# Kernel optimization log

Hardware: AMD Instinct MI355X
Metric: run time of the kernel (lower is better)

## Reference

```python
import jax, jax.numpy as jnp
import numpy as np

NEG_SLOPE = 0.2  # PyG GATConv default negative_slope
H, C = 4, 64     # heads, per-head channels


def gat_layer(x, src, dst, edge_attr, W, a_src, a_dst, We, a_e, b):
    """PyG-style GATConv with edge features, concat=True. src/dst include self loops."""
    N = x.shape[0]
    h = (x @ W).reshape(N, H, C)                      # [N,H,C]
    al_s = (h * a_src[None]).sum(-1)                  # [N,H]
    al_d = (h * a_dst[None]).sum(-1)                  # [N,H]
    eh = (edge_attr @ We).reshape(-1, H, C)           # [E,H,C]
    al_e = (eh * a_e[None]).sum(-1)                   # [E,H]
    alpha = jax.nn.leaky_relu(al_s[src] + al_d[dst] + al_e, NEG_SLOPE)  # [E,H]
    # softmax over incoming edges of each destination node
    m = jax.ops.segment_max(alpha, dst, num_segments=N)
    p = jnp.exp(alpha - m[dst])
    denom = jax.ops.segment_sum(p, dst, num_segments=N)
    w = p / (denom[dst] + 1e-16)                      # [E,H]
    msg = h[src] * w[..., None]                       # [E,H,C]
    out = jax.ops.segment_sum(msg, dst, num_segments=N)  # [N,H,C]
    return out.reshape(N, H * C) + b


def setup_inputs() -> dict:
    key = jax.random.key(0)
    ks = jax.random.split(key, 20)
    N, E = 50000, 800000
    s = 0.05
    inp = {
        'x': jax.random.normal(ks[0], (N, 5), jnp.float32),
        'edge_index': jax.random.randint(ks[1], (2, E), 0, N, jnp.int32),
        'edge_attr': jax.random.normal(ks[2], (E, 4), jnp.float32),
        'W0': jax.random.normal(ks[3], (5, 256), jnp.float32) * s,
        'a_src0': jax.random.normal(ks[4], (H, C), jnp.float32) * s,
        'a_dst0': jax.random.normal(ks[5], (H, C), jnp.float32) * s,
        'We0': jax.random.normal(ks[6], (4, 256), jnp.float32) * s,
        'a_e0': jax.random.normal(ks[7], (H, C), jnp.float32) * s,
        'b0': jnp.zeros((256,), jnp.float32),
        'W1': jax.random.normal(ks[8], (256, 256), jnp.float32) * s,
        'a_src1': jax.random.normal(ks[9], (H, C), jnp.float32) * s,
        'a_dst1': jax.random.normal(ks[10], (H, C), jnp.float32) * s,
        'We1': jax.random.normal(ks[11], (4, 256), jnp.float32) * s,
        'a_e1': jax.random.normal(ks[12], (H, C), jnp.float32) * s,
        'b1': jnp.zeros((256,), jnp.float32),
        'Wm1': jax.random.normal(ks[13], (768, 128), jnp.float32) * s,
        'bm1': jnp.zeros((128,), jnp.float32),
        'Wm2': jax.random.normal(ks[14], (128, 64), jnp.float32) * s,
        'bm2': jnp.zeros((64,), jnp.float32),
        'Wm3': jax.random.normal(ks[15], (64, 128), jnp.float32) * s,
        'bm3': jnp.zeros((128,), jnp.float32),
    }
    return inp


def reference(x, edge_index, edge_attr,
              W0, a_src0, a_dst0, We0, a_e0, b0,
              W1, a_src1, a_dst1, We1, a_e1, b1,
              Wm1, bm1, Wm2, bm2, Wm3, bm3):
    N = x.shape[0]
    # add self loops once; self-loop edge_attr = mean of edge_attr (PyG fill_value='mean')
    loops = jnp.arange(N, dtype=edge_index.dtype)
    src = jnp.concatenate([edge_index[0], loops])
    dst = jnp.concatenate([edge_index[1], loops])
    mean_ea = jnp.mean(edge_attr, axis=0, keepdims=True)
    ea = jnp.concatenate([edge_attr, jnp.broadcast_to(mean_ea, (N, edge_attr.shape[1]))], axis=0)

    h = gat_layer(x, src, dst, ea, W0, a_src0, a_dst0, We0, a_e0, b0)
    h = jax.nn.relu(h)  # dropout is identity in eval
    h = gat_layer(h, src, dst, ea, W1, a_src1, a_dst1, We1, a_e1, b1)

    mean_pool = jnp.mean(h, axis=0)                      # [256]
    max_pool = jnp.max(h, axis=0)                        # [256]
    att = jax.nn.softmax(jnp.sum(h * mean_pool[None], axis=1))  # [N]
    att_pool = jnp.sum(h * att[:, None], axis=0)         # [256]
    comb = jnp.concatenate([mean_pool, max_pool, att_pool])  # [768]

    z = jax.nn.relu(comb @ Wm1 + bm1)
    z = jax.nn.relu(z @ Wm2 + bm2)
    g = z @ Wm3 + bm3
    return g[None]  # [1,128]
```

## Files before the change

kernel.cpp:

```cpp
#include <hip/hip_runtime.h>
#include <hip/hip_fp16.h>
#include <type_traits>

static const long long N_ = 50000;
static const long long E_ = 800000;

typedef __attribute__((ext_vector_type(8))) short bf16x8;
typedef __attribute__((ext_vector_type(4))) float f32x4;

__device__ __forceinline__ float lrelu(float x){ return x >= 0.f ? x : 0.2f*x; }
__device__ __forceinline__ unsigned fkey(float x){
  unsigned u = __float_as_uint(x);
  return (u & 0x80000000u) ? ~u : (u | 0x80000000u);
}
__device__ __forceinline__ float unfkey(unsigned k){
  return __uint_as_float((k & 0x80000000u) ? (k & 0x7fffffffu) : ~k);
}

__global__ void k_sumea(const float* __restrict__ ea, float* __restrict__ sum_ea){
  __shared__ float lds[256];
  int t = threadIdx.x;
  long long total = E_*4;
  float s = 0.f;
  for (long long i = (long long)blockIdx.x*256 + t; i < total; i += (long long)gridDim.x*256)
    s += ea[i];
  lds[t] = s; __syncthreads();
  for (int st=128; st>=4; st>>=1){ if (t<st) lds[t] += lds[t+st]; __syncthreads(); }
  if (t<4) atomicAdd(&sum_ea[t], lds[t]);
}

__global__ void k_deg(const int* __restrict__ ei, int* __restrict__ deg){
  long long e = (long long)blockIdx.x*256 + threadIdx.x;
  if (e < E_) atomicAdd(&deg[ei[E_ + e]], 1);
}

__global__ void k_scan1(const int* __restrict__ deg, int* __restrict__ bsum){
  __shared__ int lds[256];
  int t = threadIdx.x;
  long long idx = (long long)blockIdx.x*256 + t;
  lds[t] = (idx < N_) ? deg[idx] : 0;
  __syncthreads();
  for (int st=128; st>=1; st>>=1){ if (t<st) lds[t] += lds[t+st]; __syncthreads(); }
  if (t==0) bsum[blockIdx.x] = lds[0];
}

__global__ void k_scan2(const int* __restrict__ bsum, int* __restrict__ bpre, int nb,
                        int* __restrict__ rowptr){
  __shared__ int lds[256];
  int t = threadIdx.x;
  int v = (t < nb) ? bsum[t] : 0;
  lds[t] = v; __syncthreads();
  for (int off=1; off<256; off<<=1){
    int add = (t>=off) ? lds[t-off] : 0;
    __syncthreads();
    lds[t] += add;
    __syncthreads();
  }
  if (t < nb) bpre[t] = lds[t] - v;
  if (t == 0) rowptr[N_] = (int)E_;
}

__global__ void k_scan3(const int* __restrict__ deg, const int* __restrict__ bpre,
                        int* __restrict__ rowptr, int* __restrict__ cursor){
  __shared__ int lds[256];
  int t = threadIdx.x;
  long long idx = (long long)blockIdx.x*256 + t;
  int v = (idx < N_) ? deg[idx] : 0;
  lds[t] = v; __syncthreads();
  for (int off=1; off<256; off<<=1){
    int add = (t>=off) ? lds[t-off] : 0;
    __syncthreads();
    lds[t] += add;
    __syncthreads();
  }
  if (idx < N_){
    int rp = bpre[blockIdx.x] + lds[t] - v;
    rowptr[idx] = rp; cursor[idx] = rp;
  }
}

__global__ void k_small(const float* __restrict__ We0, const float* __restrict__ ae0,
                        const float* __restrict__ We1, const float* __restrict__ ae1,
                        const float* __restrict__ sum_ea, float* __restrict__ small){
  int t = threadIdx.x;
  if (t < 32){
    int l = t>>4, f = (t>>2)&3, h = t&3;
    const float* We = l ? We1 : We0;
    const float* ae = l ? ae1 : ae0;
    float s = 0.f;
    for (int cc=0; cc<64; cc++) s += We[f*256 + h*64 + cc]*ae[h*64+cc];
    small[l*16 + f*4 + h] = s;
  }
  __syncthreads();
  if (t < 8){
    int l = t>>2, h = t&3;
    const float* Ae = small + l*16;
    const float invE = 1.f/(float)E_;
    float s = 0.f;
    for (int f=0; f<4; f++) s += sum_ea[f]*invE*Ae[f*4+h];
    small[32 + l*4 + h] = s;
  }
}

__global__ void k_scatter(const int* __restrict__ ei, const float* __restrict__ ea,
                          int* __restrict__ cursor, int* __restrict__ csr_src,
                          float* __restrict__ ale, const float* __restrict__ small){
  long long e = (long long)blockIdx.x*256 + threadIdx.x;
  if (e >= E_) return;
  int s = ei[e], d = ei[E_+e];
  int pos = atomicAdd(&cursor[d], 1);
  csr_src[pos] = s;
  float4 v = *(const float4*)(ea + e*4);
  float o0[4], o1[4];
  #pragma unroll
  for (int h=0; h<4; h++){
    o0[h] = v.x*small[0+h]  + v.y*small[4+h]  + v.z*small[8+h]  + v.w*small[12+h];
    o1[h] = v.x*small[16+h] + v.y*small[20+h] + v.z*small[24+h] + v.w*small[28+h];
  }
  float* p = ale + (long long)pos*8;
  *(float4*)(p)   = make_float4(o0[0],o0[1],o0[2],o0[3]);
  *(float4*)(p+4) = make_float4(o1[0],o1[1],o1[2],o1[3]);
}

__global__ void k_h0(const float* __restrict__ x, const float* __restrict__ W0,
                     const float* __restrict__ as0, const float* __restrict__ ad0,
                     __half* __restrict__ h0, float* __restrict__ als, float* __restrict__ ald){
  long long wid = ((long long)blockIdx.x*blockDim.x + threadIdx.x) >> 6;
  int lane = threadIdx.x & 63;
  if (wid >= N_) return;
  const float* xr = x + wid*5;
  float xv[5];
  #pragma unroll
  for (int f=0; f<5; f++) xv[f] = xr[f];
  int c = lane*4;
  float a0=0,a1=0,a2=0,a3=0;
  #pragma unroll
  for (int f=0; f<5; f++){
    const float* wr = W0 + f*256 + c;
    a0 += xv[f]*wr[0]; a1 += xv[f]*wr[1]; a2 += xv[f]*wr[2]; a3 += xv[f]*wr[3];
  }
  __half2 p01 = __floats2half2_rn(a0,a1);
  __half2 p23 = __floats2half2_rn(a2,a3);
  uint2 pk = make_uint2(*(unsigned*)&p01, *(unsigned*)&p23);
  *(uint2*)(h0 + wid*256 + c) = pk;
  const float* asp = as0 + c;
  const float* adp = ad0 + c;
  float ss = a0*asp[0]+a1*asp[1]+a2*asp[2]+a3*asp[3];
  float dd = a0*adp[0]+a1*adp[1]+a2*adp[2]+a3*adp[3];
  int head = lane>>4;
  #pragma unroll
  for (int m=1; m<16; m<<=1){ ss += __shfl_xor(ss, m); dd += __shfl_xor(dd, m); }
  if ((lane&15)==0){ als[wid*4+head]=ss; ald[wid*4+head]=dd; }
}

template<typename OutT, bool RELU>
__global__ void k_agg(const __half* __restrict__ hin, const float* __restrict__ als,
                      const float* __restrict__ ald, const int* __restrict__ rowptr,
                      const int* __restrict__ csr_src, const float* __restrict__ ale,
                      const float* __restrict__ small, int loop_off,
                      const float* __restrict__ bias, OutT* __restrict__ out){
  long long wid = ((long long)blockIdx.x*blockDim.x + threadIdx.x) >> 6;
  int lane = threadIdx.x & 63;
  if (wid >= N_) return;
  int head = lane>>4; int c = lane*4;
  float aldv = ald[wid*4+head];
  float a0 = lrelu(als[wid*4+head] + aldv + small[loop_off+head]);
  float m = a0, d = 1.f;
  uint2 pk0 = *(const uint2*)(hin + wid*256 + c);
  float2 f01 = __half22float2(*(__half2*)&pk0.x);
  float2 f23 = __half22float2(*(__half2*)&pk0.y);
  float accx=f01.x, accy=f01.y, accz=f23.x, accw=f23.y;
  int beg = rowptr[wid], end = rowptr[wid+1];
  int i = beg;
  for (; i+1 < end; i += 2){
    int s0 = csr_src[i], s1 = csr_src[i+1];
    float a1 = lrelu(als[(long long)s0*4+head] + aldv + ale[(long long)i*8+head]);
    float a2 = lrelu(als[(long long)s1*4+head] + aldv + ale[(long long)(i+1)*8+head]);
    uint2 pku = *(const uint2*)(hin + (long long)s0*256 + c);
    uint2 pkv = *(const uint2*)(hin + (long long)s1*256 + c);
    float2 u01=__half22float2(*(__half2*)&pku.x), u23=__half22float2(*(__half2*)&pku.y);
    float2 v01=__half22float2(*(__half2*)&pkv.x), v23=__half22float2(*(__half2*)&pkv.y);
    float nm = fmaxf(m, fmaxf(a1, a2));
    float sc = __expf(m - nm);
    float p1 = __expf(a1 - nm);
    float p2 = __expf(a2 - nm);
    d = d*sc + p1 + p2;
    accx = accx*sc + p1*u01.x + p2*v01.x;
    accy = accy*sc + p1*u01.y + p2*v01.y;
    accz = accz*sc + p1*u23.x + p2*v23.x;
    accw = accw*sc + p1*u23.y + p2*v23.y;
    m = nm;
  }
  if (i < end){
    int s0 = csr_src[i];
    float a = lrelu(als[(long long)s0*4+head] + aldv + ale[(long long)i*8+head]);
    uint2 pk = *(const uint2*)(hin + (long long)s0*256 + c);
    float2 g01=__half22float2(*(__half2*)&pk.x), g23=__half22float2(*(__half2*)&pk.y);
    float nm = fmaxf(m, a);
    float sc = __expf(m - nm);
    float p  = __expf(a - nm);
    d = d*sc + p;
    accx = accx*sc + p*g01.x;
    accy = accy*sc + p*g01.y;
    accz = accz*sc + p*g23.x;
    accw = accw*sc + p*g23.y;
    m = nm;
  }
  float inv = 1.f/(d + 1e-16f);
  const float* bp = bias + c;
  float ox = accx*inv + bp[0], oy = accy*inv + bp[1];
  float oz = accz*inv + bp[2], ow = accw*inv + bp[3];
  if (RELU){ ox=fmaxf(ox,0.f); oy=fmaxf(oy,0.f); oz=fmaxf(oz,0.f); ow=fmaxf(ow,0.f); }
  if constexpr (std::is_same<OutT,__half>::value){
    __half2 q01 = __floats2half2_rn(ox,oy);
    __half2 q23 = __floats2half2_rn(oz,ow);
    uint2 qk = make_uint2(*(unsigned*)&q01, *(unsigned*)&q23);
    *(uint2*)(out + wid*256 + c) = qk;
  } else {
    *(float4*)(out + wid*256 + c) = make_float4(ox,oy,oz,ow);
  }
}

__global__ void k_prepB(const float* __restrict__ W1, ushort* __restrict__ Bhi,
                        ushort* __restrict__ Blo){
  int k = blockIdx.x;
  int n = threadIdx.x;
  float v = W1[k*256+n];
  unsigned u = __float_as_uint(v);
  ushort hi = (ushort)(u>>16);
  float rem = v - __uint_as_float(u & 0xffff0000u);
  unsigned ur = __float_as_uint(rem);
  ushort lo = (ushort)((ur + 0x7fff + ((ur>>16)&1)) >> 16);
  int t = n>>4, kb = k>>5, q = (k>>3)&3, j = k&7;
  long long idx = ((((long long)t*8+kb)*64 + q*16 + (n&15))<<3) + j;
  Bhi[idx] = hi; Blo[idx] = lo;
}

__global__ __launch_bounds__(256) void k_gemm(const float* __restrict__ A,
    const ushort* __restrict__ Bhi, const ushort* __restrict__ Blo,
    __half* __restrict__ Ch, const float* __restrict__ as1, const float* __restrict__ ad1,
    float* __restrict__ als, float* __restrict__ ald){
  __shared__ ushort Ah[32*264];
  __shared__ ushort Al[32*264];
  int t = threadIdx.x;
  long long base = (long long)blockIdx.x*32;
  for (int i=t; i<2048; i+=256){
    int r = i>>6, q4 = i&63;
    float4 v = make_float4(0.f,0.f,0.f,0.f);
    if (base + r < N_) v = *(const float4*)(A + (base+r)*256 + q4*4);
    float vv[4] = {v.x,v.y,v.z,v.w};
    ushort hh[4], ll[4];
    #pragma unroll
    for (int e=0;e<4;e++){
      unsigned u = __float_as_uint(vv[e]);
      hh[e] = (ushort)(u>>16);
      float rem = vv[e] - __uint_as_float(u & 0xffff0000u);
      unsigned ur = __float_as_uint(rem);
      ll[e] = (ushort)((ur + 0x7fff + ((ur>>16)&1)) >> 16);
    }
    int off = r*264 + q4*4;
    *(ushort4*)(Ah+off) = make_ushort4(hh[0],hh[1],hh[2],hh[3]);
    *(ushort4*)(Al+off) = make_ushort4(ll[0],ll[1],ll[2],ll[3]);
  }
  __syncthreads();
  int w = t>>6, lane = t&63, m = lane&15, q = lane>>4;
  int rbase = (w>>1)*16;
  int nhalf = (w&1)*8;
  f32x4 acc[8];
  #pragma unroll
  for (int i=0;i<8;i++) acc[i] = (f32x4){0.f,0.f,0.f,0.f};
  for (int kb=0; kb<8; kb++){
    int aoff = (rbase+m)*264 + kb*32 + q*8;
    bf16x8 ah = *(const bf16x8*)(Ah + aoff);
    bf16x8 al = *(const bf16x8*)(Al + aoff);
    #pragma unroll
    for (int tt=0; tt<8; tt++){
      long long bidx = ((((long long)(nhalf+tt)*8+kb)*64 + lane)<<3);
      bf16x8 bh = *(const bf16x8*)(Bhi + bidx);
      bf16x8 bl = *(const bf16x8*)(Blo + bidx);
      acc[tt] = __builtin_amdgcn_mfma_f32_16x16x32_bf16(ah, bh, acc[tt], 0,0,0);
      acc[tt] = __builtin_amdgcn_mfma_f32_16x16x32_bf16(al, bh, acc[tt], 0,0,0);
      acc[tt] = __builtin_amdgcn_mfma_f32_16x16x32_bf16(ah, bl, acc[tt], 0,0,0);
    }
  }
  float ssv[4][2], ddv[4][2];
  #pragma unroll
  for (int r=0;r<4;r++){ ssv[r][0]=0.f; ssv[r][1]=0.f; ddv[r][0]=0.f; ddv[r][1]=0.f; }
  #pragma unroll
  for (int tt=0; tt<8; tt++){
    int col = (nhalf+tt)*16 + m;
    float as_ = as1[col], ad_ = ad1[col];
    int hh = tt>>2;
    #pragma unroll
    for (int r=0;r<4;r++){
      ssv[r][hh] += acc[tt][r]*as_;
      ddv[r][hh] += acc[tt][r]*ad_;
    }
  }
  #pragma unroll
  for (int r=0;r<4;r++){
    #pragma unroll
    for (int hh=0; hh<2; hh++){
      #pragma unroll
      for (int mm=1; mm<16; mm<<=1){
        ssv[r][hh] += __shfl_xor(ssv[r][hh], mm);
        ddv[r][hh] += __shfl_xor(ddv[r][hh], mm);
      }
    }
  }
  #pragma unroll
  for (int r=0;r<4;r++){
    long long grow = base + rbase + q*4 + r;
    if (grow < N_){
      #pragma unroll
      for (int tt=0; tt<8; tt++)
        Ch[grow*256 + (nhalf+tt)*16 + m] = __float2half(acc[tt][r]);
      if (m==0){
        int hb = (w&1)*2;
        als[grow*4 + hb+0] = ssv[r][0];
        ald[grow*4 + hb+0] = ddv[r][0];
        als[grow*4 + hb+1] = ssv[r][1];
        ald[grow*4 + hb+1] = ddv[r][1];
      }
    }
  }
}

__global__ void k_pool1(const __half* __restrict__ h2, float* __restrict__ sum_pool,
                        unsigned* __restrict__ maxkey){
  int c = threadIdx.x;
  float s = 0.f; float m = -3.4e38f;
  for (long long n = blockIdx.x; n < N_; n += gridDim.x){
    float v = __half2float(h2[n*256+c]); s += v; m = fmaxf(m, v);
  }
  atomicAdd(&sum_pool[c], s);
  atomicMax(&maxkey[c], fkey(m));
}

__global__ void k_atts(const __half* __restrict__ h2, const float* __restrict__ sum_pool,
                       float* __restrict__ sarr, unsigned* __restrict__ smax){
  __shared__ float lmax[4];
  int t = threadIdx.x; int lane = t&63; int w = t>>6;
  const float invN = 1.f/(float)N_;
  int c = lane*4;
  float4 mp = *(const float4*)(sum_pool + c);
  float mymax = -3.4e38f;
  for (long long wid = (long long)blockIdx.x*4 + w; wid < N_; wid += (long long)gridDim.x*4){
    uint2 pk = *(const uint2*)(h2 + wid*256 + c);
    float2 a01 = __half22float2(*(__half2*)&pk.x);
    float2 a23 = __half22float2(*(__half2*)&pk.y);
    float s = (a01.x*mp.x + a01.y*mp.y + a23.x*mp.z + a23.y*mp.w)*invN;
    #pragma unroll
    for (int m=1; m<64; m<<=1) s += __shfl_xor(s, m);
    if (lane==0) sarr[wid] = s;
    mymax = fmaxf(mymax, s);
  }
  if (lane==0) lmax[w] = mymax;
  __syncthreads();
  if (t==0){
    float mm = fmaxf(fmaxf(lmax[0],lmax[1]), fmaxf(lmax[2],lmax[3]));
    atomicMax(smax, fkey(mm));
  }
}

__global__ void k_attd(const float* __restrict__ sarr, const unsigned* __restrict__ smax,
                       float* __restrict__ ssum){
  __shared__ float lds[256];
  int t = threadIdx.x;
  float mx = unfkey(*smax);
  float s = 0.f;
  for (long long i = (long long)blockIdx.x*256 + t; i < N_; i += (long long)gridDim.x*256)
    s += __expf(sarr[i] - mx);
  lds[t] = s; __syncthreads();
  for (int st=128; st>=1; st>>=1){ if (t<st) lds[t]+=lds[t+st]; __syncthreads(); }
  if (t==0) atomicAdd(ssum, lds[0]);
}

__global__ void k_attp(const __half* __restrict__ h2, const float* __restrict__ sarr,
                       const unsigned* __restrict__ smax, const float* __restrict__ ssum,
                       float* __restrict__ att_pool){
  int c = threadIdx.x;
  float mx = unfkey(*smax);
  float inv = 1.f/(*ssum);
  float acc = 0.f;
  for (long long n = blockIdx.x; n < N_; n += gridDim.x){
    float w = __expf(sarr[n]-mx)*inv;
    acc += __half2float(h2[n*256+c])*w;
  }
  atomicAdd(&att_pool[c], acc);
}

__global__ void k_mlp(const float* __restrict__ sum_pool, const unsigned* __restrict__ maxkey,
                      const float* __restrict__ att_pool,
                      const float* __restrict__ Wm1, const float* __restrict__ bm1,
                      const float* __restrict__ Wm2, const float* __restrict__ bm2,
                      const float* __restrict__ Wm3, const float* __restrict__ bm3,
                      float* __restrict__ out){
  __shared__ float comb[768];
  __shared__ float z1p[4][128]; __shared__ float z1[128];
  __shared__ float z2p[8][64];  __shared__ float z2[64];
  __shared__ float z3p[4][128];
  int t = threadIdx.x;
  const float invN = 1.f/(float)N_;
  for (int i=t; i<768; i+=512){
    float v;
    if (i < 256)      v = sum_pool[i]*invN;
    else if (i < 512) v = unfkey(maxkey[i-256]);
    else              v = att_pool[i-512];
    comb[i] = v;
  }
  __syncthreads();
  { int n = t&127, part = t>>7;
    float a = 0.f;
    for (int f=part*192; f<part*192+192; f++) a += comb[f]*Wm1[f*128+n];
    z1p[part][n] = a;
  }
  __syncthreads();
  if (t < 128)
    z1[t] = fmaxf(bm1[t] + z1p[0][t]+z1p[1][t]+z1p[2][t]+z1p[3][t], 0.f);
  __syncthreads();
  { int n = t&63, part = t>>6;
    float a = 0.f;
    for (int f=part*16; f<part*16+16; f++) a += z1[f]*Wm2[f*64+n];
    z2p[part][n] = a;
  }
  __syncthreads();
  if (t < 64){
    float a = bm2[t];
    #pragma unroll
    for (int p=0;p<8;p++) a += z2p[p][t];
    z2[t] = fmaxf(a, 0.f);
  }
  __syncthreads();
  { int n = t&127, part = t>>7;
    float a = 0.f;
    for (int f=part*16; f<part*16+16; f++) a += z2[f]*Wm3[f*128+n];
    z3p[part][n] = a;
  }
  __syncthreads();
  if (t < 128)
    out[t] = bm3[t] + z3p[0][t]+z3p[1][t]+z3p[2][t]+z3p[3][t];
}

extern "C" void kernel_launch(void* const* d_in, const int* in_sizes, int n_in,
                              void* d_out, int out_size, void* d_ws, size_t ws_size,
                              hipStream_t stream){
  (void)in_sizes; (void)n_in; (void)out_size; (void)ws_size;
  const float* x   = (const float*)d_in[0];
  const int*   ei  = (const int*)d_in[1];
  const float* ea  = (const float*)d_in[2];
  const float* W0  = (const float*)d_in[3];
  const float* as0 = (const float*)d_in[4];
  const float* ad0 = (const float*)d_in[5];
  const float* We0 = (const float*)d_in[6];
  const float* ae0 = (const float*)d_in[7];
  const float* b0  = (const float*)d_in[8];
  const float* W1  = (const float*)d_in[9];
  const float* as1 = (const float*)d_in[10];
  const float* ad1 = (const float*)d_in[11];
  const float* We1 = (const float*)d_in[12];
  const float* ae1 = (const float*)d_in[13];
  const float* b1  = (const float*)d_in[14];
  const float* Wm1 = (const float*)d_in[15];
  const float* bm1 = (const float*)d_in[16];
  const float* Wm2 = (const float*)d_in[17];
  const float* bm2 = (const float*)d_in[18];
  const float* Wm3 = (const float*)d_in[19];
  const float* bm3 = (const float*)d_in[20];
  float* out = (float*)d_out;

  char* ws = (char*)d_ws;
  size_t o = 0;
  auto alloc = [&](size_t bytes)->size_t{
    size_t r = o; o = (o + bytes + 255) & ~(size_t)255; return r;
  };
  size_t o_bufF   = alloc((size_t)N_*256*4);
  size_t o_bufH   = alloc((size_t)N_*256*2);
  size_t o_als0   = alloc((size_t)N_*4*4);
  size_t o_ald0   = alloc((size_t)N_*4*4);
  size_t o_als1   = alloc((size_t)N_*4*4);
  size_t o_ald1   = alloc((size_t)N_*4*4);
  size_t o_rowptr = alloc((size_t)(N_+1)*4);
  size_t o_cursor = alloc((size_t)N_*4);
  size_t o_csrsrc = alloc((size_t)E_*4);
  size_t o_ale    = alloc((size_t)E_*8*4);
  size_t o_sarr   = alloc((size_t)N_*4);
  size_t o_Bhi    = alloc((size_t)256*256*2);
  size_t o_Blo    = alloc((size_t)256*256*2);
  size_t o_bsum   = alloc(256*4);
  size_t o_bpre   = alloc(256*4);
  size_t zstart   = o;
  size_t o_deg    = alloc((size_t)N_*4);
  size_t o_sumea  = alloc(16);
  size_t o_sumpool= alloc(256*4);
  size_t o_maxkey = alloc(256*4);
  size_t o_attpool= alloc(256*4);
  size_t o_smax   = alloc(4);
  size_t o_ssum   = alloc(4);
  size_t zend     = o;
  size_t o_small  = alloc(40*4);

  float*  bufF   = (float*)(ws + o_bufF);
  __half* bufH   = (__half*)(ws + o_bufH);
  __half* h2h    = (__half*)(ws + o_bufF);
  float* pals0  = (float*)(ws + o_als0);
  float* pald0  = (float*)(ws + o_ald0);
  float* pals1  = (float*)(ws + o_als1);
  float* pald1  = (float*)(ws + o_ald1);
  int*   rowptr = (int*)(ws + o_rowptr);
  int*   cursor = (int*)(ws + o_cursor);
  int*   csrsrc = (int*)(ws + o_csrsrc);
  float* ale    = (float*)(ws + o_ale);
  float* sarr   = (float*)(ws + o_sarr);
  ushort* Bhi   = (ushort*)(ws + o_Bhi);
  ushort* Blo   = (ushort*)(ws + o_Blo);
  int*   bsum   = (int*)(ws + o_bsum);
  int*   bpre   = (int*)(ws + o_bpre);
  int*   deg    = (int*)(ws + o_deg);
  float* sumea  = (float*)(ws + o_sumea);
  float* sumpool= (float*)(ws + o_sumpool);
  unsigned* maxkey = (unsigned*)(ws + o_maxkey);
  float* attpool= (float*)(ws + o_attpool);
  unsigned* smax= (unsigned*)(ws + o_smax);
  float* ssum   = (float*)(ws + o_ssum);
  float* small  = (float*)(ws + o_small);

  hipMemsetAsync(ws + zstart, 0, zend - zstart, stream);

  int eb = (int)((E_ + 255)/256);
  int nb_wave = (int)((N_*64 + 255)/256);
  int gb = (int)((N_ + 31)/32);
  int sb = (int)((N_ + 255)/256);

  k_sumea  <<<1024, 256, 0, stream>>>(ea, sumea);
  k_deg    <<<eb, 256, 0, stream>>>(ei, deg);
  k_prepB  <<<256, 256, 0, stream>>>(W1, Bhi, Blo);
  k_scan1  <<<sb, 256, 0, stream>>>(deg, bsum);
  k_scan2  <<<1, 256, 0, stream>>>(bsum, bpre, sb, rowptr);
  k_scan3  <<<sb, 256, 0, stream>>>(deg, bpre, rowptr, cursor);
  k_small  <<<1, 64, 0, stream>>>(We0, ae0, We1, ae1, sumea, small);
  k_scatter<<<eb, 256, 0, stream>>>(ei, ea, cursor, csrsrc, ale, small);
  k_h0     <<<nb_wave, 256, 0, stream>>>(x, W0, as0, ad0, bufH, pals0, pald0);
  k_agg<float,true>  <<<nb_wave, 256, 0, stream>>>(bufH, pals0, pald0, rowptr, csrsrc,
                                         ale + 0, small, 32, b0, bufF);
  k_gemm   <<<gb, 256, 0, stream>>>(bufF, Bhi, Blo, bufH, as1, ad1, pals1, pald1);
  k_agg<__half,false><<<nb_wave, 256, 0, stream>>>(bufH, pals1, pald1, rowptr, csrsrc,
                                         ale + 4, small, 36, b1, h2h);
  k_pool1  <<<256, 256, 0, stream>>>(h2h, sumpool, maxkey);
  k_atts   <<<1024, 256, 0, stream>>>(h2h, sumpool, sarr, smax);
  k_attd   <<<128, 256, 0, stream>>>(sarr, smax, ssum);
  k_attp   <<<256, 256, 0, stream>>>(h2h, sarr, smax, ssum, attpool);
  k_mlp    <<<1, 512, 0, stream>>>(sumpool, maxkey, attpool,
                                   Wm1, bm1, Wm2, bm2, Wm3, bm3, out);
}
```

Before: 585.0 us.

## Unroll aggregation by four with dual softmax accumulators, fp16 edge logits, fewer launches

The aggregation loop now processes four neighbours per iteration using two independent online-softmax accumulators, which are merged at the end. This gives more memory-level parallelism on the gathers and shortens the dependency chain. Attention logits are pre-scaled by log2(e) so exp2f can replace expf. Per-edge attention terms are stored as fp16 instead of fp32, halving that buffer's traffic. Several small setup kernels are merged into k_pre and k_scan2 to cut launch overhead, at the cost of extra registers and a slight precision loss in the edge logits.

```diff
diff --git a/kernel.cpp b/kernel.cpp
--- a/kernel.cpp
+++ b/kernel.cpp
@@ -4,6 +4,7 @@
 
 static const long long N_ = 50000;
 static const long long E_ = 800000;
+#define LOG2E 1.44269504088896f
 
 typedef __attribute__((ext_vector_type(8))) short bf16x8;
 typedef __attribute__((ext_vector_type(4))) float f32x4;
@@ -16,24 +17,36 @@
 __device__ __forceinline__ float unfkey(unsigned k){
   return __uint_as_float((k & 0x80000000u) ? (k & 0x7fffffffu) : ~k);
 }
-
-__global__ void k_sumea(const float* __restrict__ ea, float* __restrict__ sum_ea){
+__device__ __forceinline__ unsigned h2u(__half2 h){ return *(unsigned*)&h; }
+
+__global__ void k_pre(const int* __restrict__ ei, int* __restrict__ deg,
+                      const float* __restrict__ ea, float* __restrict__ sum_ea,
+                      const float* __restrict__ W1, ushort* __restrict__ Bhi,
+                      ushort* __restrict__ Blo){
+  int t = threadIdx.x;
+  long long e = (long long)blockIdx.x*256 + t;
+  if (e < E_) atomicAdd(&deg[ei[E_ + e]], 1);
+  if (blockIdx.x < 256){
+    int k = blockIdx.x, n = t;
+    float v = W1[k*256+n];
+    unsigned u = __float_as_uint(v);
+    ushort hi = (ushort)(u>>16);
+    float rem = v - __uint_as_float(u & 0xffff0000u);
+    unsigned ur = __float_as_uint(rem);
+    ushort lo = (ushort)((ur + 0x7fff + ((ur>>16)&1)) >> 16);
+    int tl = n>>4, kb = k>>5, q = (k>>3)&3, j = k&7;
+    long long idx = ((((long long)tl*8+kb)*64 + q*16 + (n&15))<<3) + j;
+    Bhi[idx] = hi; Blo[idx] = lo;
+  }
   __shared__ float lds[256];
-  int t = threadIdx.x;
-  long long total = E_*4;
   float s = 0.f;
-  for (long long i = (long long)blockIdx.x*256 + t; i < total; i += (long long)gridDim.x*256)
+  for (long long i = (long long)blockIdx.x*256 + t; i < E_*4; i += (long long)gridDim.x*256)
     s += ea[i];
   lds[t] = s; __syncthreads();
   for (int st=128; st>=4; st>>=1){ if (t<st) lds[t] += lds[t+st]; __syncthreads(); }
   if (t<4) atomicAdd(&sum_ea[t], lds[t]);
 }
 
-__global__ void k_deg(const int* __restrict__ ei, int* __restrict__ deg){
-  long long e = (long long)blockIdx.x*256 + threadIdx.x;
-  if (e < E_) atomicAdd(&deg[ei[E_ + e]], 1);
-}
-
 __global__ void k_scan1(const int* __restrict__ deg, int* __restrict__ bsum){
   __shared__ int lds[256];
   int t = threadIdx.x;
@@ -45,7 +58,10 @@
 }
 
 __global__ void k_scan2(const int* __restrict__ bsum, int* __restrict__ bpre, int nb,
-                        int* __restrict__ rowptr){
+                        int* __restrict__ rowptr,
+                        const float* __restrict__ We0, const float* __restrict__ ae0,
+                        const float* __restrict__ We1, const float* __restrict__ ae1,
+                        const float* __restrict__ sum_ea, float* __restrict__ small){
   __shared__ int lds[256];
   int t = threadIdx.x;
   int v = (t < nb) ? bsum[t] : 0;
@@ -58,6 +74,23 @@
   }
   if (t < nb) bpre[t] = lds[t] - v;
   if (t == 0) rowptr[N_] = (int)E_;
+  if (t < 32){
+    int l = t>>4, f = (t>>2)&3, h = t&3;
+    const float* We = l ? We1 : We0;
+    const float* ae = l ? ae1 : ae0;
+    float s = 0.f;
+    for (int cc=0; cc<64; cc++) s += We[f*256 + h*64 + cc]*ae[h*64+cc];
+    small[l*16 + f*4 + h] = s * LOG2E;
+  }
+  __syncthreads();
+  if (t < 8){
+    int l = t>>2, h = t&3;
+    const float* Ae = small + l*16;
+    const float invE = 1.f/(float)E_;
+    float s = 0.f;
+    for (int f=0; f<4; f++) s += sum_ea[f]*invE*Ae[f*4+h];
+    small[32 + l*4 + h] = s;
+  }
 }
 
 __global__ void k_scan3(const int* __restrict__ deg, const int* __restrict__ bpre,
@@ -79,32 +112,9 @@
   }
 }
 
-__global__ void k_small(const float* __restrict__ We0, const float* __restrict__ ae0,
-                        const float* __restrict__ We1, const float* __restrict__ ae1,
-                        const float* __restrict__ sum_ea, float* __restrict__ small){
-  int t = threadIdx.x;
-  if (t < 32){
-    int l = t>>4, f = (t>>2)&3, h = t&3;
-    const float* We = l ? We1 : We0;
-    const float* ae = l ? ae1 : ae0;
-    float s = 0.f;
-    for (int cc=0; cc<64; cc++) s += We[f*256 + h*64 + cc]*ae[h*64+cc];
-    small[l*16 + f*4 + h] = s;
-  }
-  __syncthreads();
-  if (t < 8){
-    int l = t>>2, h = t&3;
-    const float* Ae = small + l*16;
-    const float invE = 1.f/(float)E_;
-    float s = 0.f;
-    for (int f=0; f<4; f++) s += sum_ea[f]*invE*Ae[f*4+h];
-    small[32 + l*4 + h] = s;
-  }
-}
-
 __global__ void k_scatter(const int* __restrict__ ei, const float* __restrict__ ea,
                           int* __restrict__ cursor, int* __restrict__ csr_src,
-                          float* __restrict__ ale, const float* __restrict__ small){
+                          __half* __restrict__ aleh, const float* __restrict__ small){
   long long e = (long long)blockIdx.x*256 + threadIdx.x;
   if (e >= E_) return;
   int s = ei[e], d = ei[E_+e];
@@ -117,17 +127,19 @@
     o0[h] = v.x*small[0+h]  + v.y*small[4+h]  + v.z*small[8+h]  + v.w*small[12+h];
     o1[h] = v.x*small[16+h] + v.y*small[20+h] + v.z*small[24+h] + v.w*small[28+h];
   }
-  float* p = ale + (long long)pos*8;
-  *(float4*)(p)   = make_float4(o0[0],o0[1],o0[2],o0[3]);
-  *(float4*)(p+4) = make_float4(o1[0],o1[1],o1[2],o1[3]);
+  uint4 pk = make_uint4(h2u(__floats2half2_rn(o0[0],o0[1])),
+                        h2u(__floats2half2_rn(o0[2],o0[3])),
+                        h2u(__floats2half2_rn(o1[0],o1[1])),
+                        h2u(__floats2half2_rn(o1[2],o1[3])));
+  *(uint4*)(aleh + (long long)pos*8) = pk;
 }
 
 __global__ void k_h0(const float* __restrict__ x, const float* __restrict__ W0,
                      const float* __restrict__ as0, const float* __restrict__ ad0,
                      __half* __restrict__ h0, float* __restrict__ als, float* __restrict__ ald){
-  long long wid = ((long long)blockIdx.x*blockDim.x + threadIdx.x) >> 6;
+  int wid = (int)(((long long)blockIdx.x*blockDim.x + threadIdx.x) >> 6);
   int lane = threadIdx.x & 63;
-  if (wid >= N_) return;
+  if (wid >= (int)N_) return;
   const float* xr = x + wid*5;
   float xv[5];
   #pragma unroll
@@ -141,7 +153,7 @@
   }
   __half2 p01 = __floats2half2_rn(a0,a1);
   __half2 p23 = __floats2half2_rn(a2,a3);
-  uint2 pk = make_uint2(*(unsigned*)&p01, *(unsigned*)&p23);
+  uint2 pk = make_uint2(h2u(p01), h2u(p23));
   *(uint2*)(h0 + wid*256 + c) = pk;
   const float* asp = as0 + c;
   const float* adp = ad0 + c;
@@ -150,90 +162,99 @@
   int head = lane>>4;
   #pragma unroll
   for (int m=1; m<16; m<<=1){ ss += __shfl_xor(ss, m); dd += __shfl_xor(dd, m); }
-  if ((lane&15)==0){ als[wid*4+head]=ss; ald[wid*4+head]=dd; }
+  if ((lane&15)==0){ als[wid*4+head]=ss*LOG2E; ald[wid*4+head]=dd*LOG2E; }
 }
 
 template<typename OutT, bool RELU>
-__global__ void k_agg(const __half* __restrict__ hin, const float* __restrict__ als,
-                      const float* __restrict__ ald, const int* __restrict__ rowptr,
-                      const int* __restrict__ csr_src, const float* __restrict__ ale,
-                      const float* __restrict__ small, int loop_off,
-                      const float* __restrict__ bias, OutT* __restrict__ out){
-  long long wid = ((long long)blockIdx.x*blockDim.x + threadIdx.x) >> 6;
+__global__ __launch_bounds__(256) void k_agg(const __half* __restrict__ hin,
+    const float* __restrict__ als, const float* __restrict__ ald,
+    const int* __restrict__ rowptr, const int* __restrict__ csr_src,
+    const __half* __restrict__ aleh,
+    const float* __restrict__ small, int loop_off,
+    const float* __restrict__ bias, OutT* __restrict__ out){
+  int wid = (int)(((long long)blockIdx.x*256 + threadIdx.x) >> 6);
   int lane = threadIdx.x & 63;
-  if (wid >= N_) return;
-  int head = lane>>4; int c = lane*4;
+  if (wid >= (int)N_) return;
+  int head = lane>>4, c = lane*4;
+  const uint2* hp = (const uint2*)hin;
   float aldv = ald[wid*4+head];
-  float a0 = lrelu(als[wid*4+head] + aldv + small[loop_off+head]);
-  float m = a0, d = 1.f;
-  uint2 pk0 = *(const uint2*)(hin + wid*256 + c);
+  float aS = lrelu(als[wid*4+head] + aldv + small[loop_off+head]);
+  float mA = aS, dA = 1.f;
+  uint2 pk0 = hp[wid*64 + lane];
   float2 f01 = __half22float2(*(__half2*)&pk0.x);
   float2 f23 = __half22float2(*(__half2*)&pk0.y);
-  float accx=f01.x, accy=f01.y, accz=f23.x, accw=f23.y;
+  float aAx=f01.x, aAy=f01.y, aAz=f23.x, aAw=f23.y;
+  float mB=-1e30f, dB=0.f, aBx=0.f, aBy=0.f, aBz=0.f, aBw=0.f;
   int beg = rowptr[wid], end = rowptr[wid+1];
   int i = beg;
-  for (; i+1 < end; i += 2){
-    int s0 = csr_src[i], s1 = csr_src[i+1];
-    float a1 = lrelu(als[(long long)s0*4+head] + aldv + ale[(long long)i*8+head]);
-    float a2 = lrelu(als[(long long)s1*4+head] + aldv + ale[(long long)(i+1)*8+head]);
-    uint2 pku = *(const uint2*)(hin + (long long)s0*256 + c);
-    uint2 pkv = *(const uint2*)(hin + (long long)s1*256 + c);
-    float2 u01=__half22float2(*(__half2*)&pku.x), u23=__half22float2(*(__half2*)&pku.y);
-    float2 v01=__half22float2(*(__half2*)&pkv.x), v23=__half22float2(*(__half2*)&pkv.y);
-    float nm = fmaxf(m, fmaxf(a1, a2));
-    float sc = __expf(m - nm);
-    float p1 = __expf(a1 - nm);
-    float p2 = __expf(a2 - nm);
-    d = d*sc + p1 + p2;
-    accx = accx*sc + p1*u01.x + p2*v01.x;
-    accy = accy*sc + p1*u01.y + p2*v01.y;
-    accz = accz*sc + p1*u23.x + p2*v23.x;
-    accw = accw*sc + p1*u23.y + p2*v23.y;
-    m = nm;
-  }
-  if (i < end){
+  for (; i+3 < end; i+=4){
+    int s0=csr_src[i], s1=csr_src[i+1], s2=csr_src[i+2], s3=csr_src[i+3];
+    float t0=als[s0*4+head], t1=als[s1*4+head];
+    float t2=als[s2*4+head], t3=als[s3*4+head];
+    float e0=__half2float(aleh[i*8+head]);
+    float e1=__half2float(aleh[(i+1)*8+head]);
+    float e2=__half2float(aleh[(i+2)*8+head]);
+    float e3=__half2float(aleh[(i+3)*8+head]);
+    uint2 r0=hp[s0*64+lane], r1=hp[s1*64+lane];
+    uint2 r2=hp[s2*64+lane], r3=hp[s3*64+lane];
+    float a0=lrelu(t0+aldv+e0), a1=lrelu(t1+aldv+e1);
+    float a2=lrelu(t2+aldv+e2), a3=lrelu(t3+aldv+e3);
+    {
+      float nm = fmaxf(mA, fmaxf(a0,a1));
+      float sc = exp2f(mA-nm), p0 = exp2f(a0-nm), p1 = exp2f(a1-nm);
+      float2 u01=__half22float2(*(__half2*)&r0.x), u23=__half22float2(*(__half2*)&r0.y);
+      float2 v01=__half22float2(*(__half2*)&r1.x), v23=__half22float2(*(__half2*)&r1.y);
+      dA  = dA*sc + p0 + p1;
+      aAx = aAx*sc + p0*u01.x + p1*v01.x;
+      aAy = aAy*sc + p0*u01.y + p1*v01.y;
+      aAz = aAz*sc + p0*u23.x + p1*v23.x;
+      aAw = aAw*sc + p0*u23.y + p1*v23.y;
+      mA = nm;
+    }
+    {
+      float nm = fmaxf(mB, fmaxf(a2,a3));
+      float sc = exp2f(mB-nm), p2 = exp2f(a2-nm), p3 = exp2f(a3-nm);
+      float2 u01=__half22float2(*(__half2*)&r2.x), u23=__half22float2(*(__half2*)&r2.y);
+      float2 v01=__half22float2(*(__half2*)&r3.x), v23=__half22float2(*(__half2*)&r3.y);
+      dB  = dB*sc + p2 + p3;
+      aBx = aBx*sc + p2*u01.x + p3*v01.x;
+      aBy = aBy*sc + p2*u01.y + p3*v01.y;
+      aBz = aBz*sc + p2*u23.x + p3*v23.x;
+      aBw = aBw*sc + p2*u23.y + p3*v23.y;
+      mB = nm;
+    }
+  }
+  for (; i < end; i++){
     int s0 = csr_src[i];
-    float a = lrelu(als[(long long)s0*4+head] + aldv + ale[(long long)i*8+head]);
-    uint2 pk = *(const uint2*)(hin + (long long)s0*256 + c);
-    float2 g01=__half22float2(*(__half2*)&pk.x), g23=__half22float2(*(__half2*)&pk.y);
-    float nm = fmaxf(m, a);
-    float sc = __expf(m - nm);
-    float p  = __expf(a - nm);
-    d = d*sc + p;
-    accx = accx*sc + p*g01.x;
-    accy = accy*sc + p*g01.y;
-    accz = accz*sc + p*g23.x;
-    accw = accw*sc + p*g23.y;
-    m = nm;
-  }
+    float e0 = __half2float(aleh[i*8+head]);
+    float a = lrelu(als[s0*4+head] + aldv + e0);
+    uint2 r = hp[s0*64+lane];
+    float nm = fmaxf(mA, a);
+    float sc = exp2f(mA-nm), p = exp2f(a-nm);
+    float2 g01=__half22float2(*(__half2*)&r.x), g23=__half22float2(*(__half2*)&r.y);
+    dA  = dA*sc + p;
+    aAx = aAx*sc + p*g01.x;
+    aAy = aAy*sc + p*g01.y;
+    aAz = aAz*sc + p*g23.x;
+    aAw = aAw*sc + p*g23.y;
+    mA = nm;
+  }
+  float nm = fmaxf(mA, mB);
+  float sA = exp2f(mA-nm), sB = exp2f(mB-nm);
+  float d  = dA*sA + dB*sB;
+  float ax = aAx*sA + aBx*sB, ay = aAy*sA + aBy*sB;
+  float az = aAz*sA + aBz*sB, aw = aAw*sA + aBw*sB;
   float inv = 1.f/(d + 1e-16f);
   const float* bp = bias + c;
-  float ox = accx*inv + bp[0], oy = accy*inv + bp[1];
-  float oz = accz*inv + bp[2], ow = accw*inv + bp[3];
+  float ox = ax*inv + bp[0], oy = ay*inv + bp[1];
+  float oz = az*inv + bp[2], ow = aw*inv + bp[3];
   if (RELU){ ox=fmaxf(ox,0.f); oy=fmaxf(oy,0.f); oz=fmaxf(oz,0.f); ow=fmaxf(ow,0.f); }
   if constexpr (std::is_same<OutT,__half>::value){
-    __half2 q01 = __floats2half2_rn(ox,oy);
-    __half2 q23 = __floats2half2_rn(oz,ow);
-    uint2 qk = make_uint2(*(unsigned*)&q01, *(unsigned*)&q23);
+    uint2 qk = make_uint2(h2u(__floats2half2_rn(ox,oy)), h2u(__floats2half2_rn(oz,ow)));
     *(uint2*)(out + wid*256 + c) = qk;
   } else {
     *(float4*)(out + wid*256 + c) = make_float4(ox,oy,oz,ow);
   }
-}
-
-__global__ void k_prepB(const float* __restrict__ W1, ushort* __restrict__ Bhi,
-                        ushort* __restrict__ Blo){
-  int k = blockIdx.x;
-  int n = threadIdx.x;
-  float v = W1[k*256+n];
-  unsigned u = __float_as_uint(v);
-  ushort hi = (ushort)(u>>16);
-  float rem = v - __uint_as_float(u & 0xffff0000u);
-  unsigned ur = __float_as_uint(rem);
-  ushort lo = (ushort)((ur + 0x7fff + ((ur>>16)&1)) >> 16);
-  int t = n>>4, kb = k>>5, q = (k>>3)&3, j = k&7;
-  long long idx = ((((long long)t*8+kb)*64 + q*16 + (n&15))<<3) + j;
-  Bhi[idx] = hi; Blo[idx] = lo;
 }
 
 __global__ __launch_bounds__(256) void k_gemm(const float* __restrict__ A,
@@ -317,10 +338,10 @@
         Ch[grow*256 + (nhalf+tt)*16 + m] = __float2half(acc[tt][r]);
       if (m==0){
         int hb = (w&1)*2;
-        als[grow*4 + hb+0] = ssv[r][0];
-        ald[grow*4 + hb+0] = ddv[r][0];
-        als[grow*4 + hb+1] = ssv[r][1];
-        ald[grow*4 + hb+1] = ddv[r][1];
+        als[grow*4 + hb+0] = ssv[r][0]*LOG2E;
+        ald[grow*4 + hb+0] = ddv[r][0]*LOG2E;
+        als[grow*4 + hb+1] = ssv[r][1]*LOG2E;
+        ald[grow*4 + hb+1] = ddv[r][1]*LOG2E;
       }
     }
   }
@@ -483,7 +504,7 @@
   size_t o_rowptr = alloc((size_t)(N_+1)*4);
   size_t o_cursor = alloc((size_t)N_*4);
   size_t o_csrsrc = alloc((size_t)E_*4);
-  size_t o_ale    = alloc((size_t)E_*8*4);
+  size_t o_ale    = alloc((size_t)E_*8*2);
   size_t o_sarr   = alloc((size_t)N_*4);
   size_t o_Bhi    = alloc((size_t)256*256*2);
   size_t o_Blo    = alloc((size_t)256*256*2);
@@ -510,7 +531,7 @@
   int*   rowptr = (int*)(ws + o_rowptr);
   int*   cursor = (int*)(ws + o_cursor);
   int*   csrsrc = (int*)(ws + o_csrsrc);
-  float* ale    = (float*)(ws + o_ale);
+  __half* aleh  = (__half*)(ws + o_ale);
   float* sarr   = (float*)(ws + o_sarr);
   ushort* Bhi   = (ushort*)(ws + o_Bhi);
   ushort* Blo   = (ushort*)(ws + o_Blo);
@@ -532,20 +553,18 @@
   int gb = (int)((N_ + 31)/32);
   int sb = (int)((N_ + 255)/256);
 
-  k_sumea  <<<1024, 256, 0, stream>>>(ea, sumea);
-  k_deg    <<<eb, 256, 0, stream>>>(ei, deg);
-  k_prepB  <<<256, 256, 0, stream>>>(W1, Bhi, Blo);
+  k_pre    <<<eb, 256, 0, stream>>>(ei, deg, ea, sumea, W1, Bhi, Blo);
   k_scan1  <<<sb, 256, 0, stream>>>(deg, bsum);
-  k_scan2  <<<1, 256, 0, stream>>>(bsum, bpre, sb, rowptr);
+  k_scan2  <<<1, 256, 0, stream>>>(bsum, bpre, sb, rowptr,
+                                   We0, ae0, We1, ae1, sumea, small);
   k_scan3  <<<sb, 256, 0, stream>>>(deg, bpre, rowptr, cursor);
-  k_small  <<<1, 64, 0, stream>>>(We0, ae0, We1, ae1, sumea, small);
-  k_scatter<<<eb, 256, 0, stream>>>(ei, ea, cursor, csrsrc, ale, small);
+  k_scatter<<<eb, 256, 0, stream>>>(ei, ea, cursor, csrsrc, aleh, small);
   k_h0     <<<nb_wave, 256, 0, stream>>>(x, W0, as0, ad0, bufH, pals0, pald0);
   k_agg<float,true>  <<<nb_wave, 256, 0, stream>>>(bufH, pals0, pald0, rowptr, csrsrc,
-                                         ale + 0, small, 32, b0, bufF);
+                                         aleh + 0, small, 32, b0, bufF);
   k_gemm   <<<gb, 256, 0, stream>>>(bufF, Bhi, Blo, bufH, as1, ad1, pals1, pald1);
   k_agg<__half,false><<<nb_wave, 256, 0, stream>>>(bufH, pals1, pald1, rowptr, csrsrc,
-                                         ale + 4, small, 36, b1, h2h);
+                                         aleh + 4, small, 36, b1, h2h);
   k_pool1  <<<256, 256, 0, stream>>>(h2h, sumpool, maxkey);
   k_atts   <<<1024, 256, 0, stream>>>(h2h, sumpool, sarr, smax);
   k_attd   <<<128, 256, 0, stream>>>(sarr, smax, ssum);
```

Measured after the change: 562.9 us. 3.8% less time.
